# Performance work log

Measured on AMD Instinct MI355X. Metric: run time of the kernel, lower is better.

The kernel has to match this reference:

```python
import jax, jax.numpy as jnp
import numpy as np

B, N, D = 8192, 34, 16  # batch, num fields, embedding size


def _pair_indices(n):
    # faithful to the original loop: i in [0, n-2], j in [i, n-1] (includes j == i)
    pairs = [(i, j) for i in range(n - 1) for j in range(i, n)]
    ii = np.array([p[0] for p in pairs], dtype=np.int32)
    jj = np.array([p[1] for p in pairs], dtype=np.int32)
    return ii, jj


def setup_inputs() -> dict:
    key = jax.random.key(0)
    k1, k2 = jax.random.split(key)
    x = jax.random.normal(k1, (B, N, D), dtype=jnp.float32)
    # glorot_uniform for (D, D): limit = sqrt(6 / (D + D))
    limit = np.sqrt(6.0 / (D + D)).astype(np.float32)
    W = jax.random.uniform(k2, (D, D), dtype=jnp.float32, minval=-limit, maxval=limit)
    return {"x": x, "W": W}


def reference(x, W):
    # x: [B, N, D] stacked field embeddings; W: [D, D] shared ('all' mode)
    b, n, d = x.shape
    ii, jj = _pair_indices(n)  # static index arrays, P = n*(n+1)//2 - 1 pairs
    proj = jnp.einsum('bnd,de->bne', x, W)  # project every field once
    inter = proj[:, ii, :] * x[:, jj, :]    # [B, P, D] all pairwise interactions
    return inter.reshape(b, -1)             # concat along axis 1 -> [B, P*D]
```

## Files before the change

kernel.cpp:

```cpp
#include <hip/hip_runtime.h>

#define BB 8192
#define NN 34
#define DD 16
#define PP 594

typedef float f32x4 __attribute__((ext_vector_type(4)));

struct PairTab { uchar2 v[PP]; };
constexpr PairTab make_tab() {
    PairTab t{};
    int p = 0;
    for (int i = 0; i < NN - 1; ++i)
        for (int j = i; j < NN; ++j) {
            t.v[p].x = (unsigned char)i;
            t.v[p].y = (unsigned char)j;
            ++p;
        }
    return t;
}
__device__ __constant__ PairTab c_tab = make_tab();

__global__ __launch_bounds__(256)
void BiInteraction_38577396253196_kernel(const float* __restrict__ x,
                                         const float* __restrict__ W,
                                         float* __restrict__ out)
{
    __shared__ float xs[NN * DD];
    __shared__ float ws[DD * DD];
    __shared__ float ps[NN * DD];

    const int b = blockIdx.x;
    const int t = threadIdx.x;

    const f32x4* xg = (const f32x4*)(x + (size_t)b * (NN * DD));
    if (t < 136) ((f32x4*)xs)[t] = __builtin_nontemporal_load(&xg[t]);
    if (t >= 192) ((f32x4*)ws)[t - 192] = ((const f32x4*)W)[t - 192];
    __syncthreads();

    for (int q = t; q < NN * DD; q += 256) {
        const int n = q >> 4, e = q & 15;
        float acc = 0.f;
#pragma unroll
        for (int d = 0; d < DD; ++d)
            acc = fmaf(xs[n * DD + d], ws[d * DD + e], acc);
        ps[q] = acc;
    }
    __syncthreads();

    f32x4* og = (f32x4*)(out + (size_t)b * (PP * DD));
    const f32x4* psv = (const f32x4*)ps;
    const f32x4* xsv = (const f32x4*)xs;
#pragma unroll
    for (int it = 0; it < 9; ++it) {
        const int k4 = t + it * 256;
        const int p = k4 >> 2, d4 = k4 & 3;
        const uchar2 pr = c_tab.v[p];
        const f32x4 r = psv[pr.x * 4 + d4] * xsv[pr.y * 4 + d4];
        __builtin_nontemporal_store(r, &og[k4]);
    }
    if (t < 72) {
        const int k4 = t + 9 * 256;
        const int p = k4 >> 2, d4 = k4 & 3;
        const uchar2 pr = c_tab.v[p];
        const f32x4 r = psv[pr.x * 4 + d4] * xsv[pr.y * 4 + d4];
        __builtin_nontemporal_store(r, &og[k4]);
    }
}

extern "C" void kernel_launch(void* const* d_in, const int* in_sizes, int n_in,
                              void* d_out, int out_size, void* d_ws, size_t ws_size,
                              hipStream_t stream) {
    const float* x = (const float*)d_in[0];
    const float* W = (const float*)d_in[1];
    float* out = (float*)d_out;

    BiInteraction_38577396253196_kernel<<<BB, 256, 0, stream>>>(x, W, out);
}
```

Baseline: 69.88 us.

## Assign one batch row per wavefront with wave-level barriers instead of block syncs

Each 256-thread block now handles four batch rows, one per 64-lane wavefront, and each wave keeps a private shared-memory slice for x, the projection and its own copy of W. Block-wide __syncthreads are replaced by wave barriers, so the waves run independently and the stall while one block loads x before projecting goes away. Nontemporal loads and stores are dropped in favour of plain ones. In exchange the grid is four times smaller, each wave repeats the W copy, and per-block LDS grows about fourfold, which may reduce occupancy.

Result: faster. 68.29 us (-2.3%).

```diff
diff --git a/kernel.cpp b/kernel.cpp
--- a/kernel.cpp
+++ b/kernel.cpp
@@ -4,6 +4,8 @@
 #define NN 34
 #define DD 16
 #define PP 594
+#define XF 544
+#define NBATCH 4
 
 typedef float f32x4 __attribute__((ext_vector_type(4)));
 
@@ -26,19 +28,28 @@
                                          const float* __restrict__ W,
                                          float* __restrict__ out)
 {
-    __shared__ float xs[NN * DD];
-    __shared__ float ws[DD * DD];
-    __shared__ float ps[NN * DD];
+    __shared__ float sh[NBATCH * (XF + XF + DD * DD)];
 
-    const int b = blockIdx.x;
     const int t = threadIdx.x;
+    const int w = t >> 6, lane = t & 63;
+    const int b = blockIdx.x * NBATCH + w;
 
-    const f32x4* xg = (const f32x4*)(x + (size_t)b * (NN * DD));
-    if (t < 136) ((f32x4*)xs)[t] = __builtin_nontemporal_load(&xg[t]);
-    if (t >= 192) ((f32x4*)ws)[t - 192] = ((const f32x4*)W)[t - 192];
-    __syncthreads();
+    float* xs = sh + w * (XF + XF + DD * DD);
+    float* ps = xs + XF;
+    float* ws = ps + XF;
 
-    for (int q = t; q < NN * DD; q += 256) {
+    const f32x4* xg = (const f32x4*)(x + (size_t)b * XF);
+    f32x4* xsv = (f32x4*)xs;
+    xsv[lane]      = xg[lane];
+    xsv[lane + 64] = xg[lane + 64];
+    if (lane < 8) xsv[lane + 128] = xg[lane + 128];
+    ((f32x4*)ws)[lane] = ((const f32x4*)W)[lane];
+
+    __builtin_amdgcn_wave_barrier();
+
+#pragma unroll
+    for (int it = 0; it < 8; ++it) {
+        const int q = lane + it * 64;
         const int n = q >> 4, e = q & 15;
         float acc = 0.f;
 #pragma unroll
@@ -46,25 +57,32 @@
             acc = fmaf(xs[n * DD + d], ws[d * DD + e], acc);
         ps[q] = acc;
     }
-    __syncthreads();
+    if (lane < 32) {
+        const int q = lane + 512;
+        const int n = q >> 4, e = q & 15;
+        float acc = 0.f;
+#pragma unroll
+        for (int d = 0; d < DD; ++d)
+            acc = fmaf(xs[n * DD + d], ws[d * DD + e], acc);
+        ps[q] = acc;
+    }
+
+    __builtin_amdgcn_wave_barrier();
 
     f32x4* og = (f32x4*)(out + (size_t)b * (PP * DD));
     const f32x4* psv = (const f32x4*)ps;
-    const f32x4* xsv = (const f32x4*)xs;
-#pragma unroll
-    for (int it = 0; it < 9; ++it) {
-        const int k4 = t + it * 256;
+#pragma unroll 8
+    for (int it = 0; it < 37; ++it) {
+        const int k4 = lane + it * 64;
         const int p = k4 >> 2, d4 = k4 & 3;
         const uchar2 pr = c_tab.v[p];
-        const f32x4 r = psv[pr.x * 4 + d4] * xsv[pr.y * 4 + d4];
-        __builtin_nontemporal_store(r, &og[k4]);
+        og[k4] = psv[pr.x * 4 + d4] * xsv[pr.y * 4 + d4];
     }
-    if (t < 72) {
-        const int k4 = t + 9 * 256;
+    if (lane < 8) {
+        const int k4 = lane + 37 * 64;
         const int p = k4 >> 2, d4 = k4 & 3;
         const uchar2 pr = c_tab.v[p];
-        const f32x4 r = psv[pr.x * 4 + d4] * xsv[pr.y * 4 + d4];
-        __builtin_nontemporal_store(r, &og[k4]);
+        og[k4] = psv[pr.x * 4 + d4] * xsv[pr.y * 4 + d4];
     }
 }
 
@@ -75,5 +93,5 @@
     const float* W = (const float*)d_in[1];
     float* out = (float*)d_out;
 
-    BiInteraction_38577396253196_kernel<<<BB, 256, 0, stream>>>(x, W, out);
+    BiInteraction_38577396253196_kernel<<<BB / NBATCH, 256, 0, stream>>>(x, W, out);
 }
```

## Split work per wavefront by field ranges to replace block barriers with wave barriers

Applied to the files above, without the earlier changes.

Each of the four wavefronts now loads the full x row and W into shared memory itself, projects only the field rows its pair range needs, and writes its own contiguous range of pairs. This swaps the block-wide __syncthreads for wave-local barriers, removing cross-wave synchronisation. The cost is that x and W are loaded redundantly by every wave. The output stores also change from nontemporal to regular stores, and the work split across waves is unequal.

Result: no change. 69.17 us (-1.0%).

```diff
diff --git a/kernel.cpp b/kernel.cpp
--- a/kernel.cpp
+++ b/kernel.cpp
@@ -4,6 +4,7 @@
 #define NN 34
 #define DD 16
 #define PP 594
+#define XF 544
 
 typedef float f32x4 __attribute__((ext_vector_type(4)));
 
@@ -21,50 +22,56 @@
 }
 __device__ __constant__ PairTab c_tab = make_tab();
 
+
 __global__ __launch_bounds__(256)
 void BiInteraction_38577396253196_kernel(const float* __restrict__ x,
                                          const float* __restrict__ W,
                                          float* __restrict__ out)
 {
-    __shared__ float xs[NN * DD];
+    __shared__ float xs[XF];
     __shared__ float ws[DD * DD];
     __shared__ float ps[NN * DD];
 
+    const int t = threadIdx.x;
+    const int w = t >> 6, lane = t & 63;
     const int b = blockIdx.x;
-    const int t = threadIdx.x;
 
-    const f32x4* xg = (const f32x4*)(x + (size_t)b * (NN * DD));
-    if (t < 136) ((f32x4*)xs)[t] = __builtin_nontemporal_load(&xg[t]);
-    if (t >= 192) ((f32x4*)ws)[t - 192] = ((const f32x4*)W)[t - 192];
-    __syncthreads();
+    int istart, iend, pstart, pend;
+    if (w == 0)      { istart = 0;  iend = 5;  pstart = 0;   pend = 160; }
+    else if (w == 1) { istart = 5;  iend = 11; pstart = 160; pend = 319; }
+    else if (w == 2) { istart = 11; iend = 18; pstart = 319; pend = 459; }
+    else             { istart = 18; iend = 33; pstart = 459; pend = 594; }
 
-    for (int q = t; q < NN * DD; q += 256) {
-        const int n = q >> 4, e = q & 15;
+    const f32x4* xg = (const f32x4*)(x + (size_t)b * XF);
+    f32x4* xsv = (f32x4*)xs;
+    xsv[lane]      = xg[lane];
+    xsv[lane + 64] = xg[lane + 64];
+    if (lane < 8) xsv[lane + 128] = xg[lane + 128];
+    ((f32x4*)ws)[lane] = ((const f32x4*)W)[lane];
+
+    __builtin_amdgcn_wave_barrier();
+
+    const int nq = (iend - istart) * DD;
+    for (int q = lane; q < nq; q += 64) {
+        const int n = istart + (q >> 4), e = q & 15;
         float acc = 0.f;
 #pragma unroll
         for (int d = 0; d < DD; ++d)
             acc = fmaf(xs[n * DD + d], ws[d * DD + e], acc);
-        ps[q] = acc;
+        ps[n * DD + e] = acc;
     }
-    __syncthreads();
+
+    __builtin_amdgcn_wave_barrier();
 
     f32x4* og = (f32x4*)(out + (size_t)b * (PP * DD));
     const f32x4* psv = (const f32x4*)ps;
-    const f32x4* xsv = (const f32x4*)xs;
-#pragma unroll
-    for (int it = 0; it < 9; ++it) {
-        const int k4 = t + it * 256;
-        const int p = k4 >> 2, d4 = k4 & 3;
+    const int n4 = (pend - pstart) * 4;
+#pragma unroll 4
+    for (int k = lane; k < n4; k += 64) {
+        const int g = pstart * 4 + k;
+        const int p = g >> 2, d4 = g & 3;
         const uchar2 pr = c_tab.v[p];
-        const f32x4 r = psv[pr.x * 4 + d4] * xsv[pr.y * 4 + d4];
-        __builtin_nontemporal_store(r, &og[k4]);
-    }
-    if (t < 72) {
-        const int k4 = t + 9 * 256;
-        const int p = k4 >> 2, d4 = k4 & 3;
-        const uchar2 pr = c_tab.v[p];
-        const f32x4 r = psv[pr.x * 4 + d4] * xsv[pr.y * 4 + d4];
-        __builtin_nontemporal_store(r, &og[k4]);
+        og[g] = psv[pr.x * 4 + d4] * xsv[pr.y * 4 + d4];
     }
 }
 
```
